# Kernel tuning notes

Measured on AMD Instinct MI355X. Metric: run time of the kernel, lower is better.

Reference implementation:

```python
import jax, jax.numpy as jnp
import numpy as np

D_MODEL, N_HEADS, D_K, D_V = 1024, 16, 64, 64


def setup_inputs() -> dict:
    key = jax.random.key(0)
    ks = jax.random.split(key, 9)
    B, S = 8, 1024
    Q = jax.random.normal(ks[0], (B, S, D_MODEL), dtype=jnp.float32)
    K = jax.random.normal(ks[1], (B, S, D_MODEL), dtype=jnp.float32)
    V = jax.random.normal(ks[2], (B, S, D_MODEL), dtype=jnp.float32)
    # Xavier-uniform weights (gain=1): limit = sqrt(6/(fan_in+fan_out))
    lim = float(np.sqrt(6.0 / (D_MODEL + N_HEADS * D_K)))
    Wq = jax.random.uniform(ks[3], (D_MODEL, N_HEADS * D_K), minval=-lim, maxval=lim, dtype=jnp.float32)
    Wk = jax.random.uniform(ks[4], (D_MODEL, N_HEADS * D_K), minval=-lim, maxval=lim, dtype=jnp.float32)
    Wv = jax.random.uniform(ks[5], (D_MODEL, N_HEADS * D_V), minval=-lim, maxval=lim, dtype=jnp.float32)
    # nn.Linear default bias init: uniform(-1/sqrt(fan_in), 1/sqrt(fan_in))
    bl = float(1.0 / np.sqrt(D_MODEL))
    bq = jax.random.uniform(ks[6], (N_HEADS * D_K,), minval=-bl, maxval=bl, dtype=jnp.float32)
    bk = jax.random.uniform(ks[7], (N_HEADS * D_K,), minval=-bl, maxval=bl, dtype=jnp.float32)
    bv = jax.random.uniform(ks[8], (N_HEADS * D_V,), minval=-bl, maxval=bl, dtype=jnp.float32)
    return {"Q": Q, "K": K, "V": V, "Wq": Wq, "bq": bq, "Wk": Wk, "bk": bk, "Wv": Wv, "bv": bv}


def reference(Q, K, V, Wq, bq, Wk, bk, Wv, bv):
    B, S, _ = Q.shape
    # projections -> [B, H, S, d]
    q = (Q @ Wq + bq).reshape(B, S, N_HEADS, D_K).transpose(0, 2, 1, 3)
    k = (K @ Wk + bk).reshape(B, S, N_HEADS, D_K).transpose(0, 2, 1, 3)
    v = (V @ Wv + bv).reshape(B, S, N_HEADS, D_V).transpose(0, 2, 1, 3)
    scores = jnp.exp(jnp.einsum('bhqd,bhkd->bhqk', q, k) / jnp.sqrt(jnp.float32(D_K)))
    attn = scores / (jnp.sum(scores, axis=-1, keepdims=True) + 1e-8)
    ctx = jnp.einsum('bhqk,bhkd->bhqd', attn, v)  # [B,H,S,Dv]
    return ctx.transpose(0, 2, 1, 3).reshape(B, S, N_HEADS * D_V)
```

## Files before the change

kernel.cpp:

```cpp
#include <hip/hip_runtime.h>
#include <stdint.h>

#define DM 1024
#define HEADS 16
#define BATCH 8
#define SEQ 1024
#define MTOT 8192

typedef _Float16 half8 __attribute__((ext_vector_type(8)));
typedef _Float16 half4 __attribute__((ext_vector_type(4)));
typedef float floatx4 __attribute__((ext_vector_type(4)));

__device__ __forceinline__ void glds16(const void* g, void* l) {
    __builtin_amdgcn_global_load_lds(
        (const __attribute__((address_space(1))) void*)g,
        (__attribute__((address_space(3))) void*)l, 16, 0, 0);
}

__global__ __launch_bounds__(256) void prep(
        const float* __restrict__ Q, const float* __restrict__ K,
        const float* __restrict__ V,
        _Float16* __restrict__ qb, _Float16* __restrict__ kb, _Float16* __restrict__ vb,
        const float* __restrict__ Wq, const float* __restrict__ Wk,
        const float* __restrict__ Wv,
        _Float16* __restrict__ wqt, _Float16* __restrict__ wkt, _Float16* __restrict__ wvt) {
    __shared__ float t[32][33];
    int bid = blockIdx.x, tid = threadIdx.x;
    if (bid < 12288) {
        int ten = bid >> 12;
        int bx  = bid & 4095;
        const float* src = ten == 0 ? Q : (ten == 1 ? K : V);
        _Float16* dst    = ten == 0 ? qb : (ten == 1 ? kb : vb);
        size_t i = ((size_t)bx * 256 + tid) * 8;
        float4 a = *(const float4*)(src + i);
        float4 b = *(const float4*)(src + i + 4);
        half8 h;
        h[0] = (_Float16)a.x; h[1] = (_Float16)a.y; h[2] = (_Float16)a.z; h[3] = (_Float16)a.w;
        h[4] = (_Float16)b.x; h[5] = (_Float16)b.y; h[6] = (_Float16)b.z; h[7] = (_Float16)b.w;
        *(half8*)(dst + i) = h;
    } else {
        int wb = bid - 12288;
        int z  = wb >> 10;
        int rem = wb & 1023;
        const float* W = z == 0 ? Wq : (z == 1 ? Wk : Wv);
        _Float16* Wt   = z == 0 ? wqt : (z == 1 ? wkt : wvt);
        int k0 = (rem & 31) * 32, n0 = (rem >> 5) * 32;
        int tx = tid & 31, ty = tid >> 5;
#pragma unroll
        for (int i = 0; i < 4; i++)
            t[ty + i * 8][tx] = W[(size_t)(k0 + ty + i * 8) * DM + n0 + tx];
        __syncthreads();
#pragma unroll
        for (int i = 0; i < 4; i++)
            Wt[(size_t)(n0 + ty + i * 8) * DM + k0 + tx] = (_Float16)t[tx][ty + i * 8];
    }
}

__global__ __launch_bounds__(256) void proj_gemm(
        const _Float16* __restrict__ qb, const _Float16* __restrict__ kb,
        const _Float16* __restrict__ vb,
        const _Float16* __restrict__ wqt, const _Float16* __restrict__ wkt,
        const _Float16* __restrict__ wvt,
        const float* __restrict__ bq, const float* __restrict__ bk,
        const float* __restrict__ bv,
        _Float16* __restrict__ qh, _Float16* __restrict__ kh, _Float16* __restrict__ vT) {
    __shared__ _Float16 As[2][128 * 64];
    __shared__ _Float16 Bs[2][128 * 64];
    int z = blockIdx.z;
    const _Float16* A  = z == 0 ? qb : (z == 1 ? kb : vb);
    const _Float16* Bw = z == 0 ? wqt : (z == 1 ? wkt : wvt);
    const float* bias  = z == 0 ? bq : (z == 1 ? bk : bv);
    int m0 = blockIdx.x * 128, n0 = blockIdx.y * 128;
    int tid = threadIdx.x, wid = tid >> 6, lane = tid & 63;
    int l15 = lane & 15, quad = lane >> 4;
    int wm = wid >> 1, wn = wid & 1;
    bool swapped = (z < 2);

    int rbase = wid * 32 + (lane >> 3);
    int pg = (lane & 7) ^ (lane >> 3);

    floatx4 acc[4][4] = {};

#pragma unroll
    for (int ii = 0; ii < 4; ii++) {
        int rr = rbase + ii * 8;
        glds16(A  + (size_t)(m0 + rr) * DM + pg * 8, &As[0][(wid * 4 + ii) * 512]);
        glds16(Bw + (size_t)(n0 + rr) * DM + pg * 8, &Bs[0][(wid * 4 + ii) * 512]);
    }
    __syncthreads();

    for (int t = 0; t < 16; t++) {
        int cur = t & 1;

        if (t < 15) {
            int k0 = (t + 1) * 64;
#pragma unroll
            for (int ii = 0; ii < 4; ii++) {
                int rr = rbase + ii * 8;
                glds16(A  + (size_t)(m0 + rr) * DM + k0 + pg * 8,
                       &As[cur ^ 1][(wid * 4 + ii) * 512]);
                glds16(Bw + (size_t)(n0 + rr) * DM + k0 + pg * 8,
                       &Bs[cur ^ 1][(wid * 4 + ii) * 512]);
            }
        }

#pragma unroll
        for (int kc = 0; kc < 2; kc++) {
            half8 a[4], b[4];
#pragma unroll
            for (int mt = 0; mt < 4; mt++) {
                int row = wm * 64 + mt * 16 + l15;
                int pl = (kc * 4 + quad) ^ (l15 & 7);
                a[mt] = *(const half8*)&As[cur][row * 64 + pl * 8];
            }
#pragma unroll
            for (int nt = 0; nt < 4; nt++) {
                int row = wn * 64 + nt * 16 + l15;
                int pl = (kc * 4 + quad) ^ (l15 & 7);
                b[nt] = *(const half8*)&Bs[cur][row * 64 + pl * 8];
            }
            if (swapped) {
#pragma unroll
                for (int mt = 0; mt < 4; mt++)
#pragma unroll
                    for (int nt = 0; nt < 4; nt++)
                        acc[mt][nt] = __builtin_amdgcn_mfma_f32_16x16x32_f16(
                            b[nt], a[mt], acc[mt][nt], 0, 0, 0);
            } else {
#pragma unroll
                for (int mt = 0; mt < 4; mt++)
#pragma unroll
                    for (int nt = 0; nt < 4; nt++)
                        acc[mt][nt] = __builtin_amdgcn_mfma_f32_16x16x32_f16(
                            a[mt], b[nt], acc[mt][nt], 0, 0, 0);
            }
        }

        __syncthreads();
    }

    if (swapped) {
        float sc = (z == 0) ? 0.125f : 1.0f;
        _Float16* out = (z == 0) ? qh : kh;
#pragma unroll
        for (int nt = 0; nt < 4; nt++) {
            int d0 = n0 + wn * 64 + nt * 16 + quad * 4;
            int hh = d0 >> 6, dd = d0 & 63;
            floatx4 b4 = *(const floatx4*)&bias[d0];
#pragma unroll
            for (int mt = 0; mt < 4; mt++) {
                int s = m0 + wm * 64 + mt * 16 + l15;
                int b_ = s >> 10, ss = s & 1023;
                size_t off = ((size_t)(b_ * HEADS + hh)) * 65536 + (size_t)ss * 64 + dd;
                half4 hv;
#pragma unroll
                for (int r = 0; r < 4; r++)
                    hv[r] = (_Float16)((acc[mt][nt][r] + b4[r]) * sc);
                *(half4*)&out[off] = hv;
            }
        }
    } else {
#pragma unroll
        for (int nt = 0; nt < 4; nt++) {
            int d = n0 + wn * 64 + nt * 16 + l15;
            int hh = d >> 6, dd = d & 63;
            float bv_ = bias[d];
#pragma unroll
            for (int mt = 0; mt < 4; mt++) {
                int s0 = m0 + wm * 64 + mt * 16 + quad * 4;
                int b_ = s0 >> 10, ss = s0 & 1023;
                size_t off = ((size_t)(b_ * HEADS + hh)) * 65536 + (size_t)dd * 1024 + ss;
                half4 hv;
#pragma unroll
                for (int r = 0; r < 4; r++)
                    hv[r] = (_Float16)(acc[mt][nt][r] + bv_);
                *(half4*)&vT[off] = hv;
            }
        }
    }
}

__global__ __launch_bounds__(256) void attn(
        const _Float16* __restrict__ qh, const _Float16* __restrict__ kh,
        const _Float16* __restrict__ vT, float* __restrict__ out) {
    __shared__ _Float16 Ks[4096];
    __shared__ _Float16 Vs[4096];
    __shared__ _Float16 QP[16384];
    int qt = blockIdx.x, h = blockIdx.y, b = blockIdx.z;
    size_t base = ((size_t)(b * HEADS + h)) * 65536;
    int tid = threadIdx.x, wid = tid >> 6, lane = tid & 63;
    int l15 = lane & 15, quad = lane >> 4;
    int rs = lane >> 3;
    int pg = (lane & 7) ^ rs;

#pragma unroll
    for (int ii = 0; ii < 8; ii++) {
        int issue = wid * 8 + ii;
        int r = issue * 8 + rs;
        glds16(qh + base + (size_t)(qt * 256 + r) * 64 + pg * 8, &QP[issue * 512]);
    }
    __syncthreads();
    half8 qf[4][2];
#pragma unroll
    for (int mt = 0; mt < 4; mt++)
#pragma unroll
        for (int kc = 0; kc < 2; kc++) {
            int row = wid * 64 + mt * 16 + l15;
            int pl = (kc * 4 + quad) ^ (l15 & 7);
            qf[mt][kc] = *(const half8*)&QP[row * 64 + pl * 8];
        }
    __syncthreads();

    floatx4 oacc[4][4] = {};
    float rden[4] = {0.f, 0.f, 0.f, 0.f};
    _Float16* Pw = &QP[wid * 4096];

    for (int kt = 0; kt < 16; kt++) {
        __syncthreads();
#pragma unroll
        for (int ii = 0; ii < 2; ii++) {
            int issue = wid * 2 + ii;
            int r = issue * 8 + rs;
            glds16(kh + base + (size_t)(kt * 64 + r) * 64 + pg * 8, &Ks[issue * 512]);
            glds16(vT + base + (size_t)r * 1024 + kt * 64 + pg * 8, &Vs[issue * 512]);
        }
        __syncthreads();

#pragma unroll
        for (int hf = 0; hf < 2; hf++) {
            floatx4 sacc[2][4] = {};
#pragma unroll
            for (int kc = 0; kc < 2; kc++) {
                half8 kf[2];
#pragma unroll
                for (int kn2 = 0; kn2 < 2; kn2++) {
                    int kn = hf * 2 + kn2;
                    int pl = (kc * 4 + quad) ^ (l15 & 7);
                    kf[kn2] = *(const half8*)&Ks[(kn * 16 + l15) * 64 + pl * 8];
                }
#pragma unroll
                for (int kn2 = 0; kn2 < 2; kn2++)
#pragma unroll
                    for (int mt = 0; mt < 4; mt++)
                        sacc[kn2][mt] = __builtin_amdgcn_mfma_f32_16x16x32_f16(
                            kf[kn2], qf[mt][kc], sacc[kn2][mt], 0, 0, 0);
            }
#pragma unroll
            for (int kn2 = 0; kn2 < 2; kn2++) {
                int kn = hf * 2 + kn2;
#pragma unroll
                for (int mt = 0; mt < 4; mt++) {
                    half4 ph;
#pragma unroll
                    for (int r = 0; r < 4; r++) {
                        float p = __expf(sacc[kn2][mt][r]);
                        rden[mt] += p;
                        ph[r] = (_Float16)p;
                    }
                    *(half4*)&Pw[(kn * 2 + (quad >> 1)) * 512 + (mt * 16 + l15) * 8 +
                                 (quad & 1) * 4] = ph;
                }
            }
            half8 af[4], vf[4];
#pragma unroll
            for (int mt = 0; mt < 4; mt++)
                af[mt] = *(const half8*)&Pw[(hf * 4 + quad) * 512 + (mt * 16 + l15) * 8];
#pragma unroll
            for (int dn = 0; dn < 4; dn++) {
                int pl = (hf * 4 + quad) ^ (l15 & 7);
                vf[dn] = *(const half8*)&Vs[(dn * 16 + l15) * 64 + pl * 8];
            }
#pragma unroll
            for (int mt = 0; mt < 4; mt++)
#pragma unroll
                for (int dn = 0; dn < 4; dn++)
                    oacc[mt][dn] = __builtin_amdgcn_mfma_f32_16x16x32_f16(
                        af[mt], vf[dn], oacc[mt][dn], 0, 0, 0);
        }
    }

#pragma unroll
    for (int mt = 0; mt < 4; mt++) {
        float d = rden[mt];
        d += __shfl_xor(d, 16, 64);
        d += __shfl_xor(d, 32, 64);
        rden[mt] = 1.0f / (d + 1e-8f);
    }
#pragma unroll
    for (int mt = 0; mt < 4; mt++) {
#pragma unroll
        for (int r = 0; r < 4; r++) {
            float dinv = __shfl(rden[mt], quad * 4 + r, 16);
            int s = qt * 256 + wid * 64 + mt * 16 + quad * 4 + r;
#pragma unroll
            for (int dn = 0; dn < 4; dn++) {
                int col = h * 64 + dn * 16 + l15;
                out[((size_t)(b * SEQ + s)) * 1024 + col] = oacc[mt][dn][r] * dinv;
            }
        }
    }
}

extern "C" void kernel_launch(void* const* d_in, const int* in_sizes, int n_in,
                              void* d_out, int out_size, void* d_ws, size_t ws_size,
                              hipStream_t stream) {
    const float* Q  = (const float*)d_in[0];
    const float* K  = (const float*)d_in[1];
    const float* V  = (const float*)d_in[2];
    const float* Wq = (const float*)d_in[3];
    const float* bq = (const float*)d_in[4];
    const float* Wk = (const float*)d_in[5];
    const float* bk = (const float*)d_in[6];
    const float* Wv = (const float*)d_in[7];
    const float* bv = (const float*)d_in[8];
    float* out = (float*)d_out;

    char* ws = (char*)d_ws;
    const size_t TEN = (size_t)MTOT * DM * sizeof(_Float16);
    _Float16* qb  = (_Float16*)(ws);
    _Float16* kb  = (_Float16*)(ws + TEN);
    _Float16* vb  = (_Float16*)(ws + 2 * TEN);
    _Float16* qh  = (_Float16*)(ws + 3 * TEN);
    _Float16* kh  = (_Float16*)(ws + 4 * TEN);
    _Float16* vT  = (_Float16*)(ws + 5 * TEN);
    const size_t WTN = (size_t)DM * DM * sizeof(_Float16);
    _Float16* wqt = (_Float16*)(ws + 6 * TEN);
    _Float16* wkt = (_Float16*)(ws + 6 * TEN + WTN);
    _Float16* wvt = (_Float16*)(ws + 6 * TEN + 2 * WTN);

    prep<<<dim3(15360), 256, 0, stream>>>(Q, K, V, qb, kb, vb,
                                          Wq, Wk, Wv, wqt, wkt, wvt);
    proj_gemm<<<dim3(64, 8, 3), 256, 0, stream>>>(qb, kb, vb, wqt, wkt, wvt,
                                                  bq, bk, bv, qh, kh, vT);
    attn<<<dim3(4, 16, 8), 256, 0, stream>>>(qh, kh, vT, out);
}
```

Before: 276.7 us.

## Enlarge projection GEMM tile to 256x128 and double-buffer attention K/V tiles

```diff
diff --git a/kernel.cpp b/kernel.cpp
--- a/kernel.cpp
+++ b/kernel.cpp
@@ -56,7 +56,7 @@
     }
 }
 
-__global__ __launch_bounds__(256) void proj_gemm(
+__global__ __launch_bounds__(512) void proj_gemm(
         const _Float16* __restrict__ qb, const _Float16* __restrict__ kb,
         const _Float16* __restrict__ vb,
         const _Float16* __restrict__ wqt, const _Float16* __restrict__ wkt,
@@ -64,28 +64,32 @@
         const float* __restrict__ bq, const float* __restrict__ bk,
         const float* __restrict__ bv,
         _Float16* __restrict__ qh, _Float16* __restrict__ kh, _Float16* __restrict__ vT) {
-    __shared__ _Float16 As[2][128 * 64];
+    __shared__ _Float16 As[2][256 * 64];
     __shared__ _Float16 Bs[2][128 * 64];
     int z = blockIdx.z;
     const _Float16* A  = z == 0 ? qb : (z == 1 ? kb : vb);
     const _Float16* Bw = z == 0 ? wqt : (z == 1 ? wkt : wvt);
     const float* bias  = z == 0 ? bq : (z == 1 ? bk : bv);
-    int m0 = blockIdx.x * 128, n0 = blockIdx.y * 128;
+    int m0 = blockIdx.x * 256, n0 = blockIdx.y * 128;
     int tid = threadIdx.x, wid = tid >> 6, lane = tid & 63;
     int l15 = lane & 15, quad = lane >> 4;
     int wm = wid >> 1, wn = wid & 1;
     bool swapped = (z < 2);
 
-    int rbase = wid * 32 + (lane >> 3);
-    int pg = (lane & 7) ^ (lane >> 3);
+    int srow = lane >> 3;
+    int pg = (lane & 7) ^ srow;
 
     floatx4 acc[4][4] = {};
 
 #pragma unroll
     for (int ii = 0; ii < 4; ii++) {
-        int rr = rbase + ii * 8;
-        glds16(A  + (size_t)(m0 + rr) * DM + pg * 8, &As[0][(wid * 4 + ii) * 512]);
-        glds16(Bw + (size_t)(n0 + rr) * DM + pg * 8, &Bs[0][(wid * 4 + ii) * 512]);
+        int ia = wid * 4 + ii;
+        glds16(A + (size_t)(m0 + ia * 8 + srow) * DM + pg * 8, &As[0][ia * 512]);
+    }
+#pragma unroll
+    for (int jj = 0; jj < 2; jj++) {
+        int ib = wid * 2 + jj;
+        glds16(Bw + (size_t)(n0 + ib * 8 + srow) * DM + pg * 8, &Bs[0][ib * 512]);
     }
     __syncthreads();
 
@@ -96,11 +100,15 @@
             int k0 = (t + 1) * 64;
 #pragma unroll
             for (int ii = 0; ii < 4; ii++) {
-                int rr = rbase + ii * 8;
-                glds16(A  + (size_t)(m0 + rr) * DM + k0 + pg * 8,
-                       &As[cur ^ 1][(wid * 4 + ii) * 512]);
-                glds16(Bw + (size_t)(n0 + rr) * DM + k0 + pg * 8,
-                       &Bs[cur ^ 1][(wid * 4 + ii) * 512]);
+                int ia = wid * 4 + ii;
+                glds16(A + (size_t)(m0 + ia * 8 + srow) * DM + k0 + pg * 8,
+                       &As[cur ^ 1][ia * 512]);
+            }
+#pragma unroll
+            for (int jj = 0; jj < 2; jj++) {
+                int ib = wid * 2 + jj;
+                glds16(Bw + (size_t)(n0 + ib * 8 + srow) * DM + k0 + pg * 8,
+                       &Bs[cur ^ 1][ib * 512]);
             }
         }
 
@@ -183,8 +191,8 @@
 __global__ __launch_bounds__(256) void attn(
         const _Float16* __restrict__ qh, const _Float16* __restrict__ kh,
         const _Float16* __restrict__ vT, float* __restrict__ out) {
-    __shared__ _Float16 Ks[4096];
-    __shared__ _Float16 Vs[4096];
+    __shared__ _Float16 Ks[2][4096];
+    __shared__ _Float16 Vs[2][4096];
     __shared__ _Float16 QP[16384];
     int qt = blockIdx.x, h = blockIdx.y, b = blockIdx.z;
     size_t base = ((size_t)(b * HEADS + h)) * 65536;
@@ -199,6 +207,13 @@
         int r = issue * 8 + rs;
         glds16(qh + base + (size_t)(qt * 256 + r) * 64 + pg * 8, &QP[issue * 512]);
     }
+#pragma unroll
+    for (int ii = 0; ii < 2; ii++) {
+        int issue = wid * 2 + ii;
+        int r = issue * 8 + rs;
+        glds16(kh + base + (size_t)r * 64 + pg * 8, &Ks[0][issue * 512]);
+        glds16(vT + base + (size_t)r * 1024 + pg * 8, &Vs[0][issue * 512]);
+    }
     __syncthreads();
     half8 qf[4][2];
 #pragma unroll
@@ -216,15 +231,19 @@
     _Float16* Pw = &QP[wid * 4096];
 
     for (int kt = 0; kt < 16; kt++) {
-        __syncthreads();
-#pragma unroll
-        for (int ii = 0; ii < 2; ii++) {
-            int issue = wid * 2 + ii;
-            int r = issue * 8 + rs;
-            glds16(kh + base + (size_t)(kt * 64 + r) * 64 + pg * 8, &Ks[issue * 512]);
-            glds16(vT + base + (size_t)r * 1024 + kt * 64 + pg * 8, &Vs[issue * 512]);
-        }
-        __syncthreads();
+        int cur = kt & 1;
+
+        if (kt < 15) {
+#pragma unroll
+            for (int ii = 0; ii < 2; ii++) {
+                int issue = wid * 2 + ii;
+                int r = issue * 8 + rs;
+                glds16(kh + base + (size_t)((kt + 1) * 64 + r) * 64 + pg * 8,
+                       &Ks[cur ^ 1][issue * 512]);
+                glds16(vT + base + (size_t)r * 1024 + (kt + 1) * 64 + pg * 8,
+                       &Vs[cur ^ 1][issue * 512]);
+            }
+        }
 
 #pragma unroll
         for (int hf = 0; hf < 2; hf++) {
@@ -236,7 +255,7 @@
                 for (int kn2 = 0; kn2 < 2; kn2++) {
                     int kn = hf * 2 + kn2;
                     int pl = (kc * 4 + quad) ^ (l15 & 7);
-                    kf[kn2] = *(const half8*)&Ks[(kn * 16 + l15) * 64 + pl * 8];
+                    kf[kn2] = *(const half8*)&Ks[cur][(kn * 16 + l15) * 64 + pl * 8];
                 }
 #pragma unroll
                 for (int kn2 = 0; kn2 < 2; kn2++)
@@ -268,7 +287,7 @@
 #pragma unroll
             for (int dn = 0; dn < 4; dn++) {
                 int pl = (hf * 4 + quad) ^ (l15 & 7);
-                vf[dn] = *(const half8*)&Vs[(dn * 16 + l15) * 64 + pl * 8];
+                vf[dn] = *(const half8*)&Vs[cur][(dn * 16 + l15) * 64 + pl * 8];
             }
 #pragma unroll
             for (int mt = 0; mt < 4; mt++)
@@ -277,6 +296,8 @@
                     oacc[mt][dn] = __builtin_amdgcn_mfma_f32_16x16x32_f16(
                         af[mt], vf[dn], oacc[mt][dn], 0, 0, 0);
         }
+
+        __syncthreads();
     }
 
 #pragma unroll
@@ -330,7 +351,7 @@
 
     prep<<<dim3(15360), 256, 0, stream>>>(Q, K, V, qb, kb, vb,
                                           Wq, Wk, Wv, wqt, wkt, wvt);
-    proj_gemm<<<dim3(64, 8, 3), 256, 0, stream>>>(qb, kb, vb, wqt, wkt, wvt,
+    proj_gemm<<<dim3(32, 8, 3), 512, 0, stream>>>(qb, kb, vb, wqt, wkt, wvt,
                                                   bq, bk, bv, qh, kh, vT);
     attn<<<dim3(4, 16, 8), 256, 0, stream>>>(qh, kh, vT, out);
 }
```

New measurement: 285.9 us. +3.3%, slower.
